# Performance work log

Measured on AMD Instinct MI355X. Metric: run time of the kernel, lower is better.

The kernel has to match this reference:

```python
import jax, jax.numpy as jnp
import numpy as np

N, D, C, K, M = 32768, 512, 64, 16, 128
DEPTH = 4            # log2(K): decision-tree depth per codebook
NODES = K - 1        # 15 internal tree nodes per codebook


def _build_selection_matrix():
    # Node i of the binary tree lives at level log2(i+1) and thresholds the
    # level-l selected dimension of its codebook.
    S = np.zeros((C * NODES, C * DEPTH), dtype=np.float32)
    base = np.zeros((NODES, DEPTH), dtype=np.float32)
    for i in range(NODES):
        base[i, int(np.log2(i + 1))] = 1.0
    for c in range(C):
        S[c * NODES:(c + 1) * NODES, c * DEPTH:(c + 1) * DEPTH] = base
    return S


def _build_bit_matrix():
    # Leaf k scores +1/-1 on each of its DEPTH ancestor nodes; the true leaf
    # attains the maximal score DEPTH.
    base = np.zeros((K, NODES), dtype=np.float32)
    for k in range(K):
        for l in range(DEPTH):
            node = (1 << l) - 1 + (k >> (DEPTH - l))   # ancestor at level l
            bit = (k >> (DEPTH - 1 - l)) & 1            # right(1)/left(0)
            base[k, node] = 1.0 if bit else -1.0
    B = np.zeros((C * K, C * NODES), dtype=np.float32)
    for c in range(C):
        B[c * K:(c + 1) * K, c * NODES:(c + 1) * NODES] = base
    return B


def setup_inputs() -> dict:
    key = jax.random.key(0)
    k1, k2, k3, k4 = jax.random.split(key, 4)
    I = jax.random.normal(k1, (N, D), jnp.float32)
    T = jax.random.normal(k2, (C * NODES,), jnp.float32) * 0.1   # thresholds
    L = jax.random.normal(k3, (M, C, K), jnp.float32)            # LUT
    dims = jnp.sort(jax.random.randint(k4, (C * DEPTH,), 0, D))  # selected cols
    S = jnp.asarray(_build_selection_matrix())
    B = jnp.asarray(_build_bit_matrix())
    temp = jnp.ones((1,), jnp.float32)
    return {"I": I, "T": T, "L": L, "S": S, "B": B, "dims": dims, "temp": temp}


def reference(I, T, L, S, B, dims, temp):
    t = temp[0]
    x_sel = I[:, dims]                                  # (N, C*DEPTH) gather
    h = x_sel @ S.T - T                                 # (N, C*NODES)
    tanh_h = jnp.tanh(h / t)
    # straight-through sign: forward sign(h), backward d(tanh(h/t))
    sign_ste = jnp.sign(h) - jax.lax.stop_gradient(tanh_h) + tanh_h
    b = sign_ste @ B.T                                  # (N, C*K) leaf scores
    soft = jax.nn.softmax(b.reshape(-1, C, K) / t, axis=2)
    hard = jax.nn.one_hot(jnp.argmax(soft, axis=2), K, dtype=soft.dtype)
    # straight-through one-hot encoding E: forward hard, backward soft
    E = hard - jax.lax.stop_gradient(soft) + soft       # (N, C, K)
    return jnp.einsum("nck,mck->nm", E, L)              # LUT gather-sum readout
```

## Files before the change

### kernel.cpp

```cpp
#include <hip/hip_runtime.h>

#define N_TOTAL 32768
#define D_DIM   512
#define C_DIM   64
#define K_DIM   16
#define M_DIM   128
#define NODES_  15
#define ROWS    16

__global__ __launch_bounds__(256) void transpose_L_kernel(
    const float* __restrict__ L, float* __restrict__ Lt)
{
    int idx = blockIdx.x * 256 + threadIdx.x;
    float v = L[idx];
    int m  = idx >> 10;
    int ck = idx & 1023;
    Lt[ck * M_DIM + m] = v;
}

__global__ __launch_bounds__(256) void halut_kernel(
    const float* __restrict__ I,
    const float* __restrict__ T,
    const int* __restrict__ dims,
    const float* __restrict__ Lt,
    float* __restrict__ out)
{
    __shared__ __align__(16) float sI[ROWS * D_DIM];
    __shared__ float sT[C_DIM * NODES_];
    __shared__ int   sDims[C_DIM * 4];
    __shared__ int   sCode[ROWS * 65];

    const int tid = threadIdx.x;
    const int n0  = blockIdx.x * ROWS;

    sDims[tid] = dims[tid];
    for (int j = tid; j < C_DIM * NODES_; j += 256)
        sT[j] = T[j];

    {
        const float4* src = (const float4*)(I + (size_t)n0 * D_DIM);
        float4* dst = (float4*)sI;
        #pragma unroll
        for (int p = 0; p < 8; ++p)
            dst[p * 256 + tid] = src[p * 256 + tid];
    }
    __syncthreads();

    for (int t = tid; t < ROWS * C_DIM; t += 256) {
        int row = t >> 6;
        int c   = t & 63;
        const float* v = sI + row * D_DIM;
        int node = 0, k = 0;
        #pragma unroll
        for (int l = 0; l < 4; ++l) {
            float h = v[sDims[(c << 2) + l]] - sT[c * NODES_ + node];
            int bit = (h > 0.0f) ? 1 : 0;
            k = (k << 1) | bit;
            node = (node << 1) + 1 + bit;
        }
        sCode[row * 65 + c] = k;
    }
    __syncthreads();

    const int r = tid >> 4;
    const int q = tid & 15;
    const int* codeRow = sCode + r * 65;

    float4 acc0 = make_float4(0.f, 0.f, 0.f, 0.f);
    float4 acc1 = make_float4(0.f, 0.f, 0.f, 0.f);

    #pragma unroll 4
    for (int c = 0; c < C_DIM; ++c) {
        int k = codeRow[c];
        const float4* lrow = (const float4*)(Lt + (((c << 4) + k) << 7) + (q << 3));
        float4 a = lrow[0];
        float4 b = lrow[1];
        acc0.x += a.x; acc0.y += a.y; acc0.z += a.z; acc0.w += a.w;
        acc1.x += b.x; acc1.y += b.y; acc1.z += b.z; acc1.w += b.w;
    }

    float4* o = (float4*)(out + (size_t)(n0 + r) * M_DIM + (q << 3));
    o[0] = acc0;
    o[1] = acc1;
}

extern "C" void kernel_launch(void* const* d_in, const int* in_sizes, int n_in,
                              void* d_out, int out_size, void* d_ws, size_t ws_size,
                              hipStream_t stream) {
    const float* I    = (const float*)d_in[0];
    const float* T    = (const float*)d_in[1];
    const float* L    = (const float*)d_in[2];
    const int*   dims = (const int*)d_in[5];

    float* Lt = (float*)d_ws;

    hipLaunchKernelGGL(transpose_L_kernel, dim3((C_DIM * K_DIM * M_DIM) / 256), dim3(256), 0, stream,
                       L, Lt);
    hipLaunchKernelGGL(halut_kernel, dim3(N_TOTAL / ROWS), dim3(256), 0, stream,
                       I, T, dims, Lt, (float*)d_out);
}
```

Baseline: 140.2 us.

## Pair codebooks into bf16 256-entry LUT and split codes/accumulate kernels

Precomputes a combined LUT where each pair of codebooks is summed over all 256 joint code combinations, stored in bf16, halving the number of gathers in the accumulation. Code computation moves into a separate kernel that packs 4-bit codes into words, and a third kernel performs the gather-sum. This cuts the number and size of LUT loads, but adds a kernel launch and a global round-trip for codes. It also introduces bf16 rounding error in the output.

```diff
diff --git a/kernel.cpp b/kernel.cpp
--- a/kernel.cpp
+++ b/kernel.cpp
@@ -8,22 +8,42 @@
 #define NODES_  15
 #define ROWS    16
 
-__global__ __launch_bounds__(256) void transpose_L_kernel(
-    const float* __restrict__ L, float* __restrict__ Lt)
+typedef unsigned short u16;
+typedef unsigned int   u32;
+
+__device__ __forceinline__ u32 f2bf_bits(float f) {
+    u32 u = __float_as_uint(f);
+    return (u + 0x7FFFu + ((u >> 16) & 1u)) >> 16;
+}
+__device__ __forceinline__ float bf_lo(u32 u) { return __uint_as_float(u << 16); }
+__device__ __forceinline__ float bf_hi(u32 u) { return __uint_as_float(u & 0xFFFF0000u); }
+
+__global__ __launch_bounds__(256) void build_lut_kernel(
+    const float* __restrict__ L, u16* __restrict__ LUT)
 {
     int idx = blockIdx.x * 256 + threadIdx.x;
-    float v = L[idx];
-    int m  = idx >> 10;
-    int ck = idx & 1023;
-    Lt[ck * M_DIM + m] = v;
+    int q  = idx & 15;
+    int kk = (idx >> 4) & 255;
+    int p  = idx >> 12;
+    int c0 = (2 * p) * 16 + (kk & 15);
+    int c1 = (2 * p + 1) * 16 + (kk >> 4);
+    u32 w[4];
+    #pragma unroll
+    for (int h = 0; h < 4; ++h) {
+        int m0 = q * 8 + 2 * h;
+        float a0 = L[m0 * 1024 + c0]       + L[m0 * 1024 + c1];
+        float a1 = L[(m0 + 1) * 1024 + c0] + L[(m0 + 1) * 1024 + c1];
+        w[h] = f2bf_bits(a0) | (f2bf_bits(a1) << 16);
+    }
+    *(uint4*)(LUT + (size_t)((p << 8) | kk) * M_DIM + q * 8) =
+        make_uint4(w[0], w[1], w[2], w[3]);
 }
 
-__global__ __launch_bounds__(256) void halut_kernel(
+__global__ __launch_bounds__(256) void codes_kernel(
     const float* __restrict__ I,
     const float* __restrict__ T,
     const int* __restrict__ dims,
-    const float* __restrict__ Lt,
-    float* __restrict__ out)
+    u32* __restrict__ codes)
 {
     __shared__ __align__(16) float sI[ROWS * D_DIM];
     __shared__ float sT[C_DIM * NODES_];
@@ -34,8 +54,7 @@
     const int n0  = blockIdx.x * ROWS;
 
     sDims[tid] = dims[tid];
-    for (int j = tid; j < C_DIM * NODES_; j += 256)
-        sT[j] = T[j];
+    for (int j = tid; j < C_DIM * NODES_; j += 256) sT[j] = T[j];
 
     {
         const float4* src = (const float4*)(I + (size_t)n0 * D_DIM);
@@ -62,21 +81,46 @@
     }
     __syncthreads();
 
+    if (tid < 128) {
+        int r = tid >> 3, w = tid & 7;
+        const int* sc = sCode + r * 65 + w * 8;
+        u32 word = 0;
+        #pragma unroll
+        for (int j = 0; j < 8; ++j) word |= ((u32)sc[j]) << (4 * j);
+        codes[(size_t)(n0 + r) * 8 + w] = word;
+    }
+}
+
+__global__ __launch_bounds__(256) void accum_kernel(
+    const u32* __restrict__ codes,
+    const u16* __restrict__ LUT,
+    float* __restrict__ out)
+{
+    __shared__ u32 sC[ROWS * 8];
+    const int tid = threadIdx.x;
+    const int n0  = blockIdx.x * ROWS;
+
+    if (tid < 128) sC[tid] = codes[(size_t)n0 * 8 + tid];
+    __syncthreads();
+
     const int r = tid >> 4;
     const int q = tid & 15;
-    const int* codeRow = sCode + r * 65;
+
+    u32 cw[8];
+    #pragma unroll
+    for (int w = 0; w < 8; ++w) cw[w] = sC[r * 8 + w];
 
     float4 acc0 = make_float4(0.f, 0.f, 0.f, 0.f);
     float4 acc1 = make_float4(0.f, 0.f, 0.f, 0.f);
 
-    #pragma unroll 4
-    for (int c = 0; c < C_DIM; ++c) {
-        int k = codeRow[c];
-        const float4* lrow = (const float4*)(Lt + (((c << 4) + k) << 7) + (q << 3));
-        float4 a = lrow[0];
-        float4 b = lrow[1];
-        acc0.x += a.x; acc0.y += a.y; acc0.z += a.z; acc0.w += a.w;
-        acc1.x += b.x; acc1.y += b.y; acc1.z += b.z; acc1.w += b.w;
+    #pragma unroll
+    for (int p = 0; p < 32; ++p) {
+        u32 kk = (cw[p >> 2] >> ((p & 3) * 8)) & 255u;
+        const uint4 v = *(const uint4*)(LUT + (size_t)(((p << 8) | kk) << 7) + (q << 3));
+        acc0.x += bf_lo(v.x); acc0.y += bf_hi(v.x);
+        acc0.z += bf_lo(v.y); acc0.w += bf_hi(v.y);
+        acc1.x += bf_lo(v.z); acc1.y += bf_hi(v.z);
+        acc1.z += bf_lo(v.w); acc1.w += bf_hi(v.w);
     }
 
     float4* o = (float4*)(out + (size_t)(n0 + r) * M_DIM + (q << 3));
@@ -92,10 +136,12 @@
     const float* L    = (const float*)d_in[2];
     const int*   dims = (const int*)d_in[5];
 
-    float* Lt = (float*)d_ws;
+    u32* codes = (u32*)d_ws;
+    u16* LUT   = (u16*)((char*)d_ws + (1 << 20));
 
-    hipLaunchKernelGGL(transpose_L_kernel, dim3((C_DIM * K_DIM * M_DIM) / 256), dim3(256), 0, stream,
-                       L, Lt);
-    hipLaunchKernelGGL(halut_kernel, dim3(N_TOTAL / ROWS), dim3(256), 0, stream,
-                       I, T, dims, Lt, (float*)d_out);
+    hipLaunchKernelGGL(build_lut_kernel, dim3(512), dim3(256), 0, stream, L, LUT);
+    hipLaunchKernelGGL(codes_kernel, dim3(N_TOTAL / ROWS), dim3(256), 0, stream,
+                       I, T, dims, codes);
+    hipLaunchKernelGGL(accum_kernel, dim3(N_TOTAL / ROWS), dim3(256), 0, stream,
+                       codes, LUT, (float*)d_out);
 }
```

Result: faster. 130.1 us (-7.2%).
